# Optimization experiments

Measured on AMD Instinct MI355X. Metric: run time of the kernel, lower is better.

## Reference

```python
import jax, jax.numpy as jnp
import numpy as np
import math

H = 12          # num_attention_heads
DH = 64         # attention_head_size
LN_EPS = 1e-5


def layer_norm(x, gamma, beta):
    mu = jnp.mean(x, axis=-1, keepdims=True)
    var = jnp.mean(jnp.square(x - mu), axis=-1, keepdims=True)
    return (x - mu) * jax.lax.rsqrt(var + LN_EPS) * gamma + beta


def setup_inputs() -> dict:
    key = jax.random.key(0)
    ks = jax.random.split(key, 12)
    B, Lq, Lk, D = 4, 512, 512, 768
    s = 1.0 / math.sqrt(D)
    return {
        "hidden_states": jax.random.normal(ks[0], (B, Lq, D), jnp.float32),
        "context": jax.random.normal(ks[1], (B, Lk, D), jnp.float32),
        "attention_mask": jnp.zeros((B, 1, 1, Lk), jnp.float32),
        "graph_arc": jax.random.randint(ks[2], (B, Lq, Lk), 0, 3, jnp.int32),
        "Wq": jax.random.normal(ks[3], (D, D), jnp.float32) * s,
        "bq": jnp.zeros((D,), jnp.float32),
        "Wk": jax.random.normal(ks[4], (D, D), jnp.float32) * s,
        "bk": jnp.zeros((D,), jnp.float32),
        "Wv": jax.random.normal(ks[5], (D, D), jnp.float32) * s,
        "bv": jnp.zeros((D,), jnp.float32),
        "dpk_emb": jax.random.normal(ks[6], (3, DH), jnp.float32),
        "dpv_emb": jax.random.normal(ks[7], (3, DH), jnp.float32),
        "lnk_g": jnp.ones((DH,), jnp.float32),
        "lnk_b": jnp.zeros((DH,), jnp.float32),
        "lnv_g": jnp.ones((DH,), jnp.float32),
        "lnv_b": jnp.zeros((DH,), jnp.float32),
    }


def reference(hidden_states, context, attention_mask, graph_arc,
              Wq, bq, Wk, bk, Wv, bv,
              dpk_emb, dpv_emb, lnk_g, lnk_b, lnv_g, lnv_b):
    B, Lq, D = hidden_states.shape
    Lk = context.shape[1]

    def heads(x, L):  # [B,L,D] -> [B,H,L,dh]
        return x.reshape(B, L, H, DH).transpose(0, 2, 1, 3)

    q = heads(hidden_states @ Wq + bq, Lq)
    k = heads(context @ Wk + bk, Lk)
    v = heads(context @ Wv + bv, Lk)

    # relation embeddings per (query, key) pair: [B,Lq,Lk,dh]
    dp_keys = layer_norm(dpk_emb[graph_arc], lnk_g, lnk_b)
    dp_values = layer_norm(dpv_emb[graph_arc], lnv_g, lnv_b)

    scores = jnp.einsum('bhqd,bhkd->bhqk', q, k) / math.sqrt(DH)
    scores = scores + jnp.einsum('bhqd,bqkd->bhqk', q, dp_keys)
    scores = scores + attention_mask
    probs = jax.nn.softmax(scores, axis=-1)  # dropout p=0.0 -> identity

    ctx = jnp.einsum('bhqk,bhkd->bhqd', probs, v)
    ctx = ctx + jnp.einsum('bhqk,bqkd->bhqd', probs, dp_values)
    ctx = ctx.transpose(0, 2, 1, 3).reshape(B, Lq, D)
    return ctx
```

## Files before the change

### kernel.cpp

```cpp
#include <hip/hip_runtime.h>
#include <hip/hip_fp16.h>

#define NB 4
#define NH 12
#define DHD 64
#define LQ 512
#define LK 512
#define DM 768

typedef __attribute__((ext_vector_type(4))) _Float16 f16x4;
typedef __attribute__((ext_vector_type(8))) _Float16 f16x8;
typedef __attribute__((ext_vector_type(4))) float f32x4;

__global__ __launch_bounds__(64) void prep_ln_kernel(
    const float* __restrict__ dpk, const float* __restrict__ dpv,
    const float* __restrict__ gk, const float* __restrict__ bk,
    const float* __restrict__ gv, const float* __restrict__ bv,
    float* __restrict__ lnK, float* __restrict__ lnV)
{
    int lane = threadIdx.x;
    for (int r = 0; r < 3; ++r) {
        {
            float x = dpk[r * DHD + lane];
            float s = x;
            #pragma unroll
            for (int o = 1; o < 64; o <<= 1) s += __shfl_xor(s, o);
            float mu = s * (1.0f / 64.0f);
            float d = x - mu;
            float v = d * d;
            #pragma unroll
            for (int o = 1; o < 64; o <<= 1) v += __shfl_xor(v, o);
            lnK[r * DHD + lane] = d * rsqrtf(v * (1.0f / 64.0f) + 1e-5f) * gk[lane] + bk[lane];
        }
        {
            float x = dpv[r * DHD + lane];
            float s = x;
            #pragma unroll
            for (int o = 1; o < 64; o <<= 1) s += __shfl_xor(s, o);
            float mu = s * (1.0f / 64.0f);
            float d = x - mu;
            float v = d * d;
            #pragma unroll
            for (int o = 1; o < 64; o <<= 1) v += __shfl_xor(v, o);
            lnV[r * DHD + lane] = d * rsqrtf(v * (1.0f / 64.0f) + 1e-5f) * gv[lane] + bv[lane];
        }
    }
}

__global__ __launch_bounds__(256) void qkv_mfma(
    const float* __restrict__ hidden, const float* __restrict__ context,
    const float* __restrict__ Wq, const float* __restrict__ bq,
    const float* __restrict__ Wk, const float* __restrict__ bk,
    const float* __restrict__ Wv, const float* __restrict__ bv,
    _Float16* __restrict__ Qh, _Float16* __restrict__ Kh,
    _Float16* __restrict__ VTh)
{
    __shared__ __align__(16) char smem[18432];
    _Float16 (*sA)[40]   = (_Float16(*)[40])smem;
    _Float16 (*sBT)[40]  = (_Float16(*)[40])(smem + 10240);
    _Float16 (*sC)[72]   = (_Float16(*)[72])smem;
    _Float16 (*sVT)[136] = (_Float16(*)[136])smem;

    const int t = threadIdx.x;
    const int w = t >> 6, lane = t & 63, g = lane >> 4, c16 = lane & 15;
    const int wm = w >> 1, wn = w & 1;
    const int mat = blockIdx.y / NH, head = blockIdx.y % NH;
    const float* X    = (mat == 0) ? hidden : context;
    const float* W    = (mat == 0) ? Wq : (mat == 1) ? Wk : Wv;
    const float* bias = (mat == 0) ? bq : (mat == 1) ? bk : bv;
    const int m0 = blockIdx.x * 128, n0 = head * DHD;

    f32x4 acc[4][2];
    #pragma unroll
    for (int mt = 0; mt < 4; ++mt)
        #pragma unroll
        for (int nt = 0; nt < 2; ++nt) acc[mt][nt] = (f32x4){0.f, 0.f, 0.f, 0.f};

    for (int kt = 0; kt < 24; ++kt) {
        __syncthreads();
        #pragma unroll
        for (int p = 0; p < 4; ++p) {
            int idx = t + p * 256;
            int row = idx >> 3, c4 = idx & 7;
            float4 xv = *(const float4*)&X[(size_t)(m0 + row) * DM + kt * 32 + c4 * 4];
            f16x4 hv = { (_Float16)xv.x, (_Float16)xv.y, (_Float16)xv.z, (_Float16)xv.w };
            *(f16x4*)&sA[row][c4 * 4] = hv;
        }
        #pragma unroll
        for (int p = 0; p < 2; ++p) {
            int idx = t + p * 256;
            int kk = idx >> 4, c4 = idx & 15;
            float4 wv = *(const float4*)&W[(size_t)(kt * 32 + kk) * DM + n0 + c4 * 4];
            sBT[c4 * 4 + 0][kk] = (_Float16)wv.x;
            sBT[c4 * 4 + 1][kk] = (_Float16)wv.y;
            sBT[c4 * 4 + 2][kk] = (_Float16)wv.z;
            sBT[c4 * 4 + 3][kk] = (_Float16)wv.w;
        }
        __syncthreads();
        f16x8 af[4], bf[2];
        #pragma unroll
        for (int mt = 0; mt < 4; ++mt)
            af[mt] = *(const f16x8*)&sA[wm * 64 + mt * 16 + c16][8 * g];
        #pragma unroll
        for (int nt = 0; nt < 2; ++nt)
            bf[nt] = *(const f16x8*)&sBT[wn * 32 + nt * 16 + c16][8 * g];
        #pragma unroll
        for (int mt = 0; mt < 4; ++mt)
            #pragma unroll
            for (int nt = 0; nt < 2; ++nt)
                acc[mt][nt] = __builtin_amdgcn_mfma_f32_16x16x32_f16(
                    af[mt], bf[nt], acc[mt][nt], 0, 0, 0);
    }

    __syncthreads();
    float bb0 = bias[n0 + wn * 32 + c16];
    float bb1 = bias[n0 + wn * 32 + 16 + c16];
    if (mat < 2) {
        #pragma unroll
        for (int mt = 0; mt < 4; ++mt)
            #pragma unroll
            for (int nt = 0; nt < 2; ++nt) {
                float bbn = nt ? bb1 : bb0;
                #pragma unroll
                for (int r = 0; r < 4; ++r) {
                    int m = wm * 64 + mt * 16 + 4 * g + r;
                    int n = wn * 32 + nt * 16 + c16;
                    sC[m][n] = (_Float16)(acc[mt][nt][r] + bbn);
                }
            }
        __syncthreads();
        _Float16* dst = (mat == 0) ? Qh : Kh;
        #pragma unroll
        for (int p = 0; p < 4; ++p) {
            int idx = t + p * 256;
            int row = idx >> 3, c8 = idx & 7;
            int m = m0 + row, bbat = m >> 9, l = m & 511;
            *(f16x8*)&dst[((size_t)(bbat * NH + head) * LQ + l) * DHD + c8 * 8] =
                *(const f16x8*)&sC[row][c8 * 8];
        }
    } else {
        #pragma unroll
        for (int mt = 0; mt < 4; ++mt)
            #pragma unroll
            for (int nt = 0; nt < 2; ++nt) {
                float bbn = nt ? bb1 : bb0;
                #pragma unroll
                for (int r = 0; r < 4; ++r) {
                    int m = wm * 64 + mt * 16 + 4 * g + r;
                    int n = wn * 32 + nt * 16 + c16;
                    sVT[n][m] = (_Float16)(acc[mt][nt][r] + bbn);
                }
            }
        __syncthreads();
        int bbat = m0 >> 9, l0 = m0 & 511;
        #pragma unroll
        for (int p = 0; p < 4; ++p) {
            int idx = t + p * 256;
            int n = idx >> 4, c8 = idx & 15;
            *(f16x8*)&VTh[((size_t)(bbat * NH + head) * DHD + n) * LK + l0 + c8 * 8] =
                *(const f16x8*)&sVT[n][c8 * 8];
        }
    }
}

__global__ __launch_bounds__(256) void attn_mfma(
    const _Float16* __restrict__ Qh, const _Float16* __restrict__ Kh,
    const _Float16* __restrict__ VTh, const float* __restrict__ maskp,
    const int* __restrict__ garc, const float* __restrict__ lnK,
    const float* __restrict__ lnV, float* __restrict__ outp)
{
    __shared__ __align__(16) _Float16 sP[16][520];
    __shared__ unsigned char sArc[16][512];
    __shared__ float sTb[16][4];
    __shared__ float sMax[4][16];
    __shared__ float sStat[4][16][4];
    __shared__ float sFin[16][4];

    const int t = threadIdx.x;
    const int w = t >> 6, lane = t & 63, g = lane >> 4, c16 = lane & 15;
    const int bx = blockIdx.x;
    const int qt = bx & 31, h = (bx >> 5) % NH, b = bx / (32 * NH);
    const int q0 = qt * 16;
    const int kw = w * 128;

    const _Float16* Qb = Qh + ((size_t)(b * NH + h) * LQ) * DHD;
    const _Float16* Kb = Kh + ((size_t)(b * NH + h) * LK) * DHD;
    const _Float16* Vb = VTh + ((size_t)(b * NH + h) * DHD) * LK;

    const int* garcRow = garc + ((size_t)(b * LQ + q0)) * LK;
    unsigned char* sArcFlat = &sArc[0][0];
    #pragma unroll
    for (int p = 0; p < 8; ++p) {
        int idx = t + p * 256;
        int4 a4 = *(const int4*)&garcRow[idx * 4];
        uchar4 u = { (unsigned char)a4.x, (unsigned char)a4.y,
                     (unsigned char)a4.z, (unsigned char)a4.w };
        *(uchar4*)&sArcFlat[idx * 4] = u;
    }
    if (t < 192) {
        int q = t / 12, rem = t % 12, rr = rem >> 2, part = rem & 3;
        float a = 0.f;
        const _Float16* qrow = Qb + (q0 + q) * DHD;
        #pragma unroll
        for (int d0 = 0; d0 < 16; ++d0) {
            int d = part * 16 + d0;
            a += (float)qrow[d] * lnK[rr * 64 + d];
        }
        a += __shfl_xor(a, 1);
        a += __shfl_xor(a, 2);
        if (part == 0) sTb[q][rr] = a;
    }
    f16x8 qa0 = *(const f16x8*)&Qb[(q0 + c16) * DHD + 8 * g];
    f16x8 qa1 = *(const f16x8*)&Qb[(q0 + c16) * DHD + 32 + 8 * g];
    __syncthreads();

    f32x4 c[8];
    int aPack[8];
    float rm[4] = {-1e30f, -1e30f, -1e30f, -1e30f};
    #pragma unroll
    for (int tt = 0; tt < 8; ++tt) {
        int kg = kw + tt * 16 + c16;
        f16x8 kb0 = *(const f16x8*)&Kb[kg * DHD + 8 * g];
        f16x8 kb1 = *(const f16x8*)&Kb[kg * DHD + 32 + 8 * g];
        f32x4 s = (f32x4){0.f, 0.f, 0.f, 0.f};
        s = __builtin_amdgcn_mfma_f32_16x16x32_f16(qa0, kb0, s, 0, 0, 0);
        s = __builtin_amdgcn_mfma_f32_16x16x32_f16(qa1, kb1, s, 0, 0, 0);
        float mv = maskp[b * LK + kg];
        int ap = 0;
        #pragma unroll
        for (int r = 0; r < 4; ++r) {
            int a = sArc[4 * g + r][kg];
            ap |= a << (8 * r);
            float sv = s[r] * 0.125f + sTb[4 * g + r][a] + mv;
            s[r] = sv;
            rm[r] = fmaxf(rm[r], sv);
        }
        c[tt] = s;
        aPack[tt] = ap;
    }

    #pragma unroll
    for (int r = 0; r < 4; ++r) {
        float m = rm[r];
        m = fmaxf(m, __shfl_xor(m, 1));
        m = fmaxf(m, __shfl_xor(m, 2));
        m = fmaxf(m, __shfl_xor(m, 4));
        m = fmaxf(m, __shfl_xor(m, 8));
        rm[r] = m;
    }
    if (c16 == 0) {
        #pragma unroll
        for (int r = 0; r < 4; ++r) sMax[w][4 * g + r] = rm[r];
    }
    __syncthreads();
    float Mr[4];
    #pragma unroll
    for (int r = 0; r < 4; ++r) {
        int q = 4 * g + r;
        Mr[r] = fmaxf(fmaxf(sMax[0][q], sMax[1][q]), fmaxf(sMax[2][q], sMax[3][q]));
    }

    float rs[4] = {0, 0, 0, 0}, b0s[4] = {0, 0, 0, 0},
          b1s[4] = {0, 0, 0, 0}, b2s[4] = {0, 0, 0, 0};
    #pragma unroll
    for (int tt = 0; tt < 8; ++tt) {
        int kg = kw + tt * 16 + c16;
        #pragma unroll
        for (int r = 0; r < 4; ++r) {
            float e = __expf(c[tt][r] - Mr[r]);
            int a = (aPack[tt] >> (8 * r)) & 255;
            rs[r] += e;
            b0s[r] += (a == 0) ? e : 0.f;
            b1s[r] += (a == 1) ? e : 0.f;
            b2s[r] += (a == 2) ? e : 0.f;
            sP[4 * g + r][kg] = (_Float16)e;
        }
    }
    #pragma unroll
    for (int r = 0; r < 4; ++r) {
        #pragma unroll
        for (int o = 1; o < 16; o <<= 1) {
            rs[r]  += __shfl_xor(rs[r], o);
            b0s[r] += __shfl_xor(b0s[r], o);
            b1s[r] += __shfl_xor(b1s[r], o);
            b2s[r] += __shfl_xor(b2s[r], o);
        }
    }
    if (c16 == 0) {
        #pragma unroll
        for (int r = 0; r < 4; ++r) {
            float4 v = make_float4(rs[r], b0s[r], b1s[r], b2s[r]);
            *(float4*)&sStat[w][4 * g + r][0] = v;
        }
    }
    __syncthreads();
    if (t < 16) {
        float4 tot = make_float4(0.f, 0.f, 0.f, 0.f);
        #pragma unroll
        for (int ww = 0; ww < 4; ++ww) {
            float4 v = *(const float4*)&sStat[ww][t][0];
            tot.x += v.x; tot.y += v.y; tot.z += v.z; tot.w += v.w;
        }
        sFin[t][0] = 1.0f / tot.x;
        sFin[t][1] = tot.y; sFin[t][2] = tot.z; sFin[t][3] = tot.w;
    }

    f32x4 o = (f32x4){0.f, 0.f, 0.f, 0.f};
    const _Float16* vrow = Vb + (size_t)(w * 16 + c16) * LK;
    #pragma unroll
    for (int ktile = 0; ktile < 16; ++ktile) {
        f16x8 pa = *(const f16x8*)&sP[c16][ktile * 32 + 8 * g];
        f16x8 vb = *(const f16x8*)&vrow[ktile * 32 + 8 * g];
        o = __builtin_amdgcn_mfma_f32_16x16x32_f16(pa, vb, o, 0, 0, 0);
    }
    __syncthreads();

    int d = w * 16 + c16;
    float lv0 = lnV[d], lv1 = lnV[64 + d], lv2 = lnV[128 + d];
    #pragma unroll
    for (int r = 0; r < 4; ++r) {
        int q = 4 * g + r;
        float4 st = *(const float4*)&sFin[q][0];
        float val = (o[r] + st.y * lv0 + st.z * lv1 + st.w * lv2) * st.x;
        outp[((size_t)(b * LQ + q0 + q)) * DM + h * DHD + d] = val;
    }
}

extern "C" void kernel_launch(void* const* d_in, const int* in_sizes, int n_in,
                              void* d_out, int out_size, void* d_ws, size_t ws_size,
                              hipStream_t stream) {
    const float* hidden  = (const float*)d_in[0];
    const float* context = (const float*)d_in[1];
    const float* mask    = (const float*)d_in[2];
    const int*   garc    = (const int*)d_in[3];
    const float* Wq = (const float*)d_in[4];
    const float* bq = (const float*)d_in[5];
    const float* Wk = (const float*)d_in[6];
    const float* bk = (const float*)d_in[7];
    const float* Wv = (const float*)d_in[8];
    const float* bv = (const float*)d_in[9];
    const float* dpk  = (const float*)d_in[10];
    const float* dpv  = (const float*)d_in[11];
    const float* lnkg = (const float*)d_in[12];
    const float* lnkb = (const float*)d_in[13];
    const float* lnvg = (const float*)d_in[14];
    const float* lnvb = (const float*)d_in[15];
    float* out = (float*)d_out;

    const size_t perT = (size_t)NB * NH * LQ * DHD;
    _Float16* Qh  = (_Float16*)d_ws;
    _Float16* Kh  = Qh + perT;
    _Float16* VTh = Kh + perT;
    float* lnK = (float*)(VTh + perT);
    float* lnV = lnK + 192;

    prep_ln_kernel<<<1, 64, 0, stream>>>(dpk, dpv, lnkg, lnkb, lnvg, lnvb, lnK, lnV);
    qkv_mfma<<<dim3(16, 36), 256, 0, stream>>>(hidden, context,
                                               Wq, bq, Wk, bk, Wv, bv,
                                               Qh, Kh, VTh);
    attn_mfma<<<1536, 256, 0, stream>>>(Qh, Kh, VTh, mask, garc, lnK, lnV, out);
}
```

Measured before the change: 163.7 us.

## Enlarge QKV GEMM and attention tiles, fold score scale into Q projection

The QKV projection now computes 128x128 output tiles (two heads per block) with a 64-wide K step, which halves the grid and the number of k-iterations and raises MFMA work per LDS load. The attention kernel processes 32 query rows per block instead of 16, so each K and V fragment loaded from global memory is reused across two query groups, halving K/V traffic and the number of blocks. The 1/sqrt(dh) scale moves into the Q projection epilogue, with the relation-key LN output pre-multiplied by 8 to compensate. Costs are higher register pressure and doubled LDS use per block, which may lower occupancy, plus one extra fp16 rounding of the pre-scaled Q.

```diff
diff --git a/kernel.cpp b/kernel.cpp
--- a/kernel.cpp
+++ b/kernel.cpp
@@ -30,7 +30,8 @@
             float v = d * d;
             #pragma unroll
             for (int o = 1; o < 64; o <<= 1) v += __shfl_xor(v, o);
-            lnK[r * DHD + lane] = d * rsqrtf(v * (1.0f / 64.0f) + 1e-5f) * gk[lane] + bk[lane];
+            lnK[r * DHD + lane] =
+                (d * rsqrtf(v * (1.0f / 64.0f) + 1e-5f) * gk[lane] + bk[lane]) * 8.0f;
         }
         {
             float x = dpv[r * DHD + lane];
@@ -55,110 +56,111 @@
     _Float16* __restrict__ Qh, _Float16* __restrict__ Kh,
     _Float16* __restrict__ VTh)
 {
-    __shared__ __align__(16) char smem[18432];
-    _Float16 (*sA)[40]   = (_Float16(*)[40])smem;
-    _Float16 (*sBT)[40]  = (_Float16(*)[40])(smem + 10240);
-    _Float16 (*sC)[72]   = (_Float16(*)[72])smem;
-    _Float16 (*sVT)[136] = (_Float16(*)[136])smem;
+    __shared__ __align__(16) char smem[36864];
+    _Float16 (*sA)[72]  = (_Float16(*)[72])smem;
+    _Float16 (*sBT)[72] = (_Float16(*)[72])(smem + 18432);
+    _Float16 (*sC)[136] = (_Float16(*)[136])smem;
 
     const int t = threadIdx.x;
     const int w = t >> 6, lane = t & 63, g = lane >> 4, c16 = lane & 15;
     const int wm = w >> 1, wn = w & 1;
-    const int mat = blockIdx.y / NH, head = blockIdx.y % NH;
+    const int mat = blockIdx.y / 6;
+    const int nt0 = blockIdx.y % 6;
     const float* X    = (mat == 0) ? hidden : context;
     const float* W    = (mat == 0) ? Wq : (mat == 1) ? Wk : Wv;
     const float* bias = (mat == 0) ? bq : (mat == 1) ? bk : bv;
-    const int m0 = blockIdx.x * 128, n0 = head * DHD;
-
-    f32x4 acc[4][2];
+    const int m0 = blockIdx.x * 128, n0 = nt0 * 128;
+    const int head0 = nt0 * 2;
+
+    f32x4 acc[4][4];
     #pragma unroll
     for (int mt = 0; mt < 4; ++mt)
         #pragma unroll
-        for (int nt = 0; nt < 2; ++nt) acc[mt][nt] = (f32x4){0.f, 0.f, 0.f, 0.f};
-
-    for (int kt = 0; kt < 24; ++kt) {
+        for (int nt = 0; nt < 4; ++nt) acc[mt][nt] = (f32x4){0.f, 0.f, 0.f, 0.f};
+
+    for (int kt = 0; kt < 12; ++kt) {
         __syncthreads();
         #pragma unroll
-        for (int p = 0; p < 4; ++p) {
+        for (int p = 0; p < 8; ++p) {
             int idx = t + p * 256;
-            int row = idx >> 3, c4 = idx & 7;
-            float4 xv = *(const float4*)&X[(size_t)(m0 + row) * DM + kt * 32 + c4 * 4];
+            int row = idx >> 4, c4 = idx & 15;
+            float4 xv = *(const float4*)&X[(size_t)(m0 + row) * DM + kt * 64 + c4 * 4];
             f16x4 hv = { (_Float16)xv.x, (_Float16)xv.y, (_Float16)xv.z, (_Float16)xv.w };
             *(f16x4*)&sA[row][c4 * 4] = hv;
         }
         #pragma unroll
-        for (int p = 0; p < 2; ++p) {
+        for (int p = 0; p < 8; ++p) {
             int idx = t + p * 256;
-            int kk = idx >> 4, c4 = idx & 15;
-            float4 wv = *(const float4*)&W[(size_t)(kt * 32 + kk) * DM + n0 + c4 * 4];
+            int kk = idx >> 5, c4 = idx & 31;
+            float4 wv = *(const float4*)&W[(size_t)(kt * 64 + kk) * DM + n0 + c4 * 4];
             sBT[c4 * 4 + 0][kk] = (_Float16)wv.x;
             sBT[c4 * 4 + 1][kk] = (_Float16)wv.y;
             sBT[c4 * 4 + 2][kk] = (_Float16)wv.z;
             sBT[c4 * 4 + 3][kk] = (_Float16)wv.w;
         }
         __syncthreads();
-        f16x8 af[4], bf[2];
+        #pragma unroll
+        for (int kh = 0; kh < 2; ++kh) {
+            f16x8 af[4], bf[4];
+            #pragma unroll
+            for (int mt = 0; mt < 4; ++mt)
+                af[mt] = *(const f16x8*)&sA[wm * 64 + mt * 16 + c16][kh * 32 + 8 * g];
+            #pragma unroll
+            for (int nt = 0; nt < 4; ++nt)
+                bf[nt] = *(const f16x8*)&sBT[wn * 64 + nt * 16 + c16][kh * 32 + 8 * g];
+            #pragma unroll
+            for (int mt = 0; mt < 4; ++mt)
+                #pragma unroll
+                for (int nt = 0; nt < 4; ++nt)
+                    acc[mt][nt] = __builtin_amdgcn_mfma_f32_16x16x32_f16(
+                        af[mt], bf[nt], acc[mt][nt], 0, 0, 0);
+        }
+    }
+
+    const float sc = (mat == 0) ? 0.125f : 1.0f;
+    float bb[4];
+    #pragma unroll
+    for (int nt = 0; nt < 4; ++nt)
+        bb[nt] = bias[n0 + wn * 64 + nt * 16 + c16] * sc;
+    __syncthreads();
+
+    if (mat < 2) {
         #pragma unroll
         for (int mt = 0; mt < 4; ++mt)
-            af[mt] = *(const f16x8*)&sA[wm * 64 + mt * 16 + c16][8 * g];
-        #pragma unroll
-        for (int nt = 0; nt < 2; ++nt)
-            bf[nt] = *(const f16x8*)&sBT[wn * 32 + nt * 16 + c16][8 * g];
-        #pragma unroll
-        for (int mt = 0; mt < 4; ++mt)
-            #pragma unroll
-            for (int nt = 0; nt < 2; ++nt)
-                acc[mt][nt] = __builtin_amdgcn_mfma_f32_16x16x32_f16(
-                    af[mt], bf[nt], acc[mt][nt], 0, 0, 0);
-    }
-
-    __syncthreads();
-    float bb0 = bias[n0 + wn * 32 + c16];
-    float bb1 = bias[n0 + wn * 32 + 16 + c16];
-    if (mat < 2) {
-        #pragma unroll
-        for (int mt = 0; mt < 4; ++mt)
-            #pragma unroll
-            for (int nt = 0; nt < 2; ++nt) {
-                float bbn = nt ? bb1 : bb0;
+            #pragma unroll
+            for (int nt = 0; nt < 4; ++nt)
                 #pragma unroll
-                for (int r = 0; r < 4; ++r) {
-                    int m = wm * 64 + mt * 16 + 4 * g + r;
-                    int n = wn * 32 + nt * 16 + c16;
-                    sC[m][n] = (_Float16)(acc[mt][nt][r] + bbn);
-                }
-            }
+                for (int r = 0; r < 4; ++r)
+                    sC[wm * 64 + mt * 16 + 4 * g + r][wn * 64 + nt * 16 + c16] =
+                        (_Float16)(acc[mt][nt][r] * sc + bb[nt]);
         __syncthreads();
         _Float16* dst = (mat == 0) ? Qh : Kh;
         #pragma unroll
-        for (int p = 0; p < 4; ++p) {
+        for (int p = 0; p < 8; ++p) {
             int idx = t + p * 256;
-            int row = idx >> 3, c8 = idx & 7;
+            int row = idx >> 4, cg = idx & 15;
+            int hl = cg >> 3, d8 = cg & 7;
             int m = m0 + row, bbat = m >> 9, l = m & 511;
-            *(f16x8*)&dst[((size_t)(bbat * NH + head) * LQ + l) * DHD + c8 * 8] =
-                *(const f16x8*)&sC[row][c8 * 8];
+            *(f16x8*)&dst[((size_t)(bbat * NH + head0 + hl) * LQ + l) * DHD + d8 * 8] =
+                *(const f16x8*)&sC[row][cg * 8];
         }
     } else {
         #pragma unroll
         for (int mt = 0; mt < 4; ++mt)
             #pragma unroll
-            for (int nt = 0; nt < 2; ++nt) {
-                float bbn = nt ? bb1 : bb0;
+            for (int nt = 0; nt < 4; ++nt)
                 #pragma unroll
-                for (int r = 0; r < 4; ++r) {
-                    int m = wm * 64 + mt * 16 + 4 * g + r;
-                    int n = wn * 32 + nt * 16 + c16;
-                    sVT[n][m] = (_Float16)(acc[mt][nt][r] + bbn);
-                }
-            }
+                for (int r = 0; r < 4; ++r)
+                    sC[wn * 64 + nt * 16 + c16][wm * 64 + mt * 16 + 4 * g + r] =
+                        (_Float16)(acc[mt][nt][r] + bb[nt]);
         __syncthreads();
         int bbat = m0 >> 9, l0 = m0 & 511;
         #pragma unroll
-        for (int p = 0; p < 4; ++p) {
+        for (int p = 0; p < 8; ++p) {
             int idx = t + p * 256;
-            int n = idx >> 4, c8 = idx & 15;
-            *(f16x8*)&VTh[((size_t)(bbat * NH + head) * DHD + n) * LK + l0 + c8 * 8] =
-                *(const f16x8*)&sVT[n][c8 * 8];
+            int n = idx >> 4, cg = idx & 15;
+            *(f16x8*)&VTh[((size_t)(bbat * NH + head0 + (n >> 6)) * DHD + (n & 63)) * LK
+                          + l0 + cg * 8] = *(const f16x8*)&sC[n][cg * 8];
         }
     }
 }
@@ -169,18 +171,18 @@
     const int* __restrict__ garc, const float* __restrict__ lnK,
     const float* __restrict__ lnV, float* __restrict__ outp)
 {
-    __shared__ __align__(16) _Float16 sP[16][520];
-    __shared__ unsigned char sArc[16][512];
-    __shared__ float sTb[16][4];
-    __shared__ float sMax[4][16];
-    __shared__ float sStat[4][16][4];
-    __shared__ float sFin[16][4];
+    __shared__ __align__(16) _Float16 sP[32][520];
+    __shared__ unsigned char sArc[32][512];
+    __shared__ float sTb[32][4];
+    __shared__ float sMax[4][32];
+    __shared__ float sStat[4][32][4];
+    __shared__ float sFin[32][4];
 
     const int t = threadIdx.x;
     const int w = t >> 6, lane = t & 63, g = lane >> 4, c16 = lane & 15;
     const int bx = blockIdx.x;
-    const int qt = bx & 31, h = (bx >> 5) % NH, b = bx / (32 * NH);
-    const int q0 = qt * 16;
+    const int qt = bx & 15, h = (bx >> 4) % NH, b = bx / (16 * NH);
+    const int q0 = qt * 32;
     const int kw = w * 128;
 
     const _Float16* Qb = Qh + ((size_t)(b * NH + h) * LQ) * DHD;
@@ -190,7 +192,7 @@
     const int* garcRow = garc + ((size_t)(b * LQ + q0)) * LK;
     unsigned char* sArcFlat = &sArc[0][0];
     #pragma unroll
-    for (int p = 0; p < 8; ++p) {
+    for (int p = 0; p < 16; ++p) {
         int idx = t + p * 256;
         int4 a4 = *(const int4*)&garcRow[idx * 4];
         uchar4 u = { (unsigned char)a4.x, (unsigned char)a4.y,
@@ -198,103 +200,130 @@
         *(uchar4*)&sArcFlat[idx * 4] = u;
     }
     if (t < 192) {
-        int q = t / 12, rem = t % 12, rr = rem >> 2, part = rem & 3;
+        int q = t / 6, rem = t % 6, rr = rem >> 1, part = rem & 1;
         float a = 0.f;
         const _Float16* qrow = Qb + (q0 + q) * DHD;
         #pragma unroll
-        for (int d0 = 0; d0 < 16; ++d0) {
-            int d = part * 16 + d0;
+        for (int d0 = 0; d0 < 32; ++d0) {
+            int d = part * 32 + d0;
             a += (float)qrow[d] * lnK[rr * 64 + d];
         }
         a += __shfl_xor(a, 1);
-        a += __shfl_xor(a, 2);
         if (part == 0) sTb[q][rr] = a;
     }
-    f16x8 qa0 = *(const f16x8*)&Qb[(q0 + c16) * DHD + 8 * g];
-    f16x8 qa1 = *(const f16x8*)&Qb[(q0 + c16) * DHD + 32 + 8 * g];
-    __syncthreads();
-
-    f32x4 c[8];
-    int aPack[8];
-    float rm[4] = {-1e30f, -1e30f, -1e30f, -1e30f};
+    f16x8 qa[2][2];
+    #pragma unroll
+    for (int qg = 0; qg < 2; ++qg) {
+        qa[qg][0] = *(const f16x8*)&Qb[(q0 + 16 * qg + c16) * DHD + 8 * g];
+        qa[qg][1] = *(const f16x8*)&Qb[(q0 + 16 * qg + c16) * DHD + 32 + 8 * g];
+    }
+    __syncthreads();
+
+    f32x4 c[8][2];
+    int aPack[8][2];
+    float rm[2][4];
+    #pragma unroll
+    for (int qg = 0; qg < 2; ++qg)
+        #pragma unroll
+        for (int r = 0; r < 4; ++r) rm[qg][r] = -1e30f;
     #pragma unroll
     for (int tt = 0; tt < 8; ++tt) {
         int kg = kw + tt * 16 + c16;
         f16x8 kb0 = *(const f16x8*)&Kb[kg * DHD + 8 * g];
         f16x8 kb1 = *(const f16x8*)&Kb[kg * DHD + 32 + 8 * g];
-        f32x4 s = (f32x4){0.f, 0.f, 0.f, 0.f};
-        s = __builtin_amdgcn_mfma_f32_16x16x32_f16(qa0, kb0, s, 0, 0, 0);
-        s = __builtin_amdgcn_mfma_f32_16x16x32_f16(qa1, kb1, s, 0, 0, 0);
         float mv = maskp[b * LK + kg];
-        int ap = 0;
-        #pragma unroll
-        for (int r = 0; r < 4; ++r) {
-            int a = sArc[4 * g + r][kg];
-            ap |= a << (8 * r);
-            float sv = s[r] * 0.125f + sTb[4 * g + r][a] + mv;
-            s[r] = sv;
-            rm[r] = fmaxf(rm[r], sv);
-        }
-        c[tt] = s;
-        aPack[tt] = ap;
-    }
-
-    #pragma unroll
-    for (int r = 0; r < 4; ++r) {
-        float m = rm[r];
-        m = fmaxf(m, __shfl_xor(m, 1));
-        m = fmaxf(m, __shfl_xor(m, 2));
-        m = fmaxf(m, __shfl_xor(m, 4));
-        m = fmaxf(m, __shfl_xor(m, 8));
-        rm[r] = m;
-    }
-    if (c16 == 0) {
-        #pragma unroll
-        for (int r = 0; r < 4; ++r) sMax[w][4 * g + r] = rm[r];
-    }
-    __syncthreads();
-    float Mr[4];
-    #pragma unroll
-    for (int r = 0; r < 4; ++r) {
-        int q = 4 * g + r;
-        Mr[r] = fmaxf(fmaxf(sMax[0][q], sMax[1][q]), fmaxf(sMax[2][q], sMax[3][q]));
-    }
-
-    float rs[4] = {0, 0, 0, 0}, b0s[4] = {0, 0, 0, 0},
-          b1s[4] = {0, 0, 0, 0}, b2s[4] = {0, 0, 0, 0};
+        #pragma unroll
+        for (int qg = 0; qg < 2; ++qg) {
+            f32x4 s = (f32x4){0.f, 0.f, 0.f, 0.f};
+            s = __builtin_amdgcn_mfma_f32_16x16x32_f16(qa[qg][0], kb0, s, 0, 0, 0);
+            s = __builtin_amdgcn_mfma_f32_16x16x32_f16(qa[qg][1], kb1, s, 0, 0, 0);
+            int ap = 0;
+            #pragma unroll
+            for (int r = 0; r < 4; ++r) {
+                int qrow = 16 * qg + 4 * g + r;
+                int a = sArc[qrow][kg];
+                ap |= a << (8 * r);
+                float sv = s[r] + sTb[qrow][a] + mv;
+                s[r] = sv;
+                rm[qg][r] = fmaxf(rm[qg][r], sv);
+            }
+            c[tt][qg] = s;
+            aPack[tt][qg] = ap;
+        }
+    }
+
+    #pragma unroll
+    for (int qg = 0; qg < 2; ++qg)
+        #pragma unroll
+        for (int r = 0; r < 4; ++r) {
+            float m = rm[qg][r];
+            m = fmaxf(m, __shfl_xor(m, 1));
+            m = fmaxf(m, __shfl_xor(m, 2));
+            m = fmaxf(m, __shfl_xor(m, 4));
+            m = fmaxf(m, __shfl_xor(m, 8));
+            rm[qg][r] = m;
+        }
+    if (c16 == 0)
+        #pragma unroll
+        for (int qg = 0; qg < 2; ++qg)
+            #pragma unroll
+            for (int r = 0; r < 4; ++r) sMax[w][16 * qg + 4 * g + r] = rm[qg][r];
+    __syncthreads();
+    float Mr[2][4];
+    #pragma unroll
+    for (int qg = 0; qg < 2; ++qg)
+        #pragma unroll
+        for (int r = 0; r < 4; ++r) {
+            int q = 16 * qg + 4 * g + r;
+            Mr[qg][r] = fmaxf(fmaxf(sMax[0][q], sMax[1][q]),
+                              fmaxf(sMax[2][q], sMax[3][q]));
+        }
+
+    float rs[2][4], b0s[2][4], b1s[2][4], b2s[2][4];
+    #pragma unroll
+    for (int qg = 0; qg < 2; ++qg)
+        #pragma unroll
+        for (int r = 0; r < 4; ++r) {
+            rs[qg][r] = 0.f; b0s[qg][r] = 0.f; b1s[qg][r] = 0.f; b2s[qg][r] = 0.f;
+        }
     #pragma unroll
     for (int tt = 0; tt < 8; ++tt) {
         int kg = kw + tt * 16 + c16;
         #pragma unroll
-        for (int r = 0; r < 4; ++r) {
-            float e = __expf(c[tt][r] - Mr[r]);
-            int a = (aPack[tt] >> (8 * r)) & 255;
-            rs[r] += e;
-            b0s[r] += (a == 0) ? e : 0.f;
-            b1s[r] += (a == 1) ? e : 0.f;
-            b2s[r] += (a == 2) ? e : 0.f;
-            sP[4 * g + r][kg] = (_Float16)e;
-        }
-    }
-    #pragma unroll
-    for (int r = 0; r < 4; ++r) {
-        #pragma unroll
-        for (int o = 1; o < 16; o <<= 1) {
-            rs[r]  += __shfl_xor(rs[r], o);
-            b0s[r] += __shfl_xor(b0s[r], o);
-            b1s[r] += __shfl_xor(b1s[r], o);
-            b2s[r] += __shfl_xor(b2s[r], o);
-        }
-    }
-    if (c16 == 0) {
-        #pragma unroll
-        for (int r = 0; r < 4; ++r) {
-            float4 v = make_float4(rs[r], b0s[r], b1s[r], b2s[r]);
-            *(float4*)&sStat[w][4 * g + r][0] = v;
-        }
-    }
-    __syncthreads();
-    if (t < 16) {
+        for (int qg = 0; qg < 2; ++qg)
+            #pragma unroll
+            for (int r = 0; r < 4; ++r) {
+                float e = __expf(c[tt][qg][r] - Mr[qg][r]);
+                int a = (aPack[tt][qg] >> (8 * r)) & 255;
+                rs[qg][r] += e;
+                b0s[qg][r] += (a == 0) ? e : 0.f;
+                b1s[qg][r] += (a == 1) ? e : 0.f;
+                b2s[qg][r] += (a == 2) ? e : 0.f;
+                sP[16 * qg + 4 * g + r][kg] = (_Float16)e;
+            }
+    }
+    #pragma unroll
+    for (int qg = 0; qg < 2; ++qg)
+        #pragma unroll
+        for (int r = 0; r < 4; ++r) {
+            #pragma unroll
+            for (int o = 1; o < 16; o <<= 1) {
+                rs[qg][r]  += __shfl_xor(rs[qg][r], o);
+                b0s[qg][r] += __shfl_xor(b0s[qg][r], o);
+                b1s[qg][r] += __shfl_xor(b1s[qg][r], o);
+                b2s[qg][r] += __shfl_xor(b2s[qg][r], o);
+            }
+        }
+    if (c16 == 0)
+        #pragma unroll
+        for (int qg = 0; qg < 2; ++qg)
+            #pragma unroll
+            for (int r = 0; r < 4; ++r) {
+                float4 v = make_float4(rs[qg][r], b0s[qg][r], b1s[qg][r], b2s[qg][r]);
+                *(float4*)&sStat[w][16 * qg + 4 * g + r][0] = v;
+            }
+    __syncthreads();
+    if (t < 32) {
         float4 tot = make_float4(0.f, 0.f, 0.f, 0.f);
         #pragma unroll
         for (int ww = 0; ww < 4; ++ww) {
@@ -305,25 +334,30 @@
         sFin[t][1] = tot.y; sFin[t][2] = tot.z; sFin[t][3] = tot.w;
     }
 
-    f32x4 o = (f32x4){0.f, 0.f, 0.f, 0.f};
+    f32x4 o[2] = {(f32x4){0.f, 0.f, 0.f, 0.f}, (f32x4){0.f, 0.f, 0.f, 0.f}};
     const _Float16* vrow = Vb + (size_t)(w * 16 + c16) * LK;
     #pragma unroll
     for (int ktile = 0; ktile < 16; ++ktile) {
-        f16x8 pa = *(const f16x8*)&sP[c16][ktile * 32 + 8 * g];
         f16x8 vb = *(const f16x8*)&vrow[ktile * 32 + 8 * g];
-        o = __builtin_amdgcn_mfma_f32_16x16x32_f16(pa, vb, o, 0, 0, 0);
+        #pragma unroll
+        for (int qg = 0; qg < 2; ++qg) {
+            f16x8 pa = *(const f16x8*)&sP[16 * qg + c16][ktile * 32 + 8 * g];
+            o[qg] = __builtin_amdgcn_mfma_f32_16x16x32_f16(pa, vb, o[qg], 0, 0, 0);
+        }
     }
     __syncthreads();
 
     int d = w * 16 + c16;
     float lv0 = lnV[d], lv1 = lnV[64 + d], lv2 = lnV[128 + d];
     #pragma unroll
-    for (int r = 0; r < 4; ++r) {
-        int q = 4 * g + r;
-        float4 st = *(const float4*)&sFin[q][0];
-        float val = (o[r] + st.y * lv0 + st.z * lv1 + st.w * lv2) * st.x;
-        outp[((size_t)(b * LQ + q0 + q)) * DM + h * DHD + d] = val;
-    }
+    for (int qg = 0; qg < 2; ++qg)
+        #pragma unroll
+        for (int r = 0; r < 4; ++r) {
+            int q = 16 * qg + 4 * g + r;
+            float4 st = *(const float4*)&sFin[q][0];
+            float val = (o[qg][r] + st.y * lv0 + st.z * lv1 + st.w * lv2) * st.x;
+            outp[((size_t)(b * LQ + q0 + q)) * DM + h * DHD + d] = val;
+        }
 }
 
 extern "C" void kernel_launch(void* const* d_in, const int* in_sizes, int n_in,
@@ -355,8 +389,8 @@
     float* lnV = lnK + 192;
 
     prep_ln_kernel<<<1, 64, 0, stream>>>(dpk, dpv, lnkg, lnkb, lnvg, lnvb, lnK, lnV);
-    qkv_mfma<<<dim3(16, 36), 256, 0, stream>>>(hidden, context,
+    qkv_mfma<<<dim3(16, 18), 256, 0, stream>>>(hidden, context,
                                                Wq, bq, Wk, bk, Wv, bv,
                                                Qh, Kh, VTh);
-    attn_mfma<<<1536, 256, 0, stream>>>(Qh, Kh, VTh, mask, garc, lnK, lnV, out);
+    attn_mfma<<<768, 256, 0, stream>>>(Qh, Kh, VTh, mask, garc, lnK, lnV, out);
 }
```

Result: slower. 184.9 us (+12.9%).
